# Kernel optimization log

Hardware: AMD Instinct MI355X
Metric: run time of the kernel (lower is better)

The kernel has to match this reference:

```python
import jax, jax.numpy as jnp
import numpy as np

D = 65
CHUNK = 64
K = 64
SCALE = D ** (-0.5)

def gelu(x):
    return jax.nn.gelu(x, approximate=False)  # torch nn.GELU default is exact erf

def setup_inputs() -> dict:
    key = jax.random.key(0)
    ks = jax.random.split(key, 16)
    B, N = 32, 16384
    s = SCALE
    return {
        "x": jax.random.normal(ks[0], (B, N, D), jnp.float32),
        # query_gen: Linear(D,D) -> GELU -> Linear(D, K*D)
        "Wq1": jax.random.normal(ks[1], (D, D), jnp.float32) * s,
        "bq1": jnp.zeros((D,), jnp.float32),
        "Wq2": jax.random.normal(ks[2], (D, K * D), jnp.float32) * s,
        "bq2": jnp.zeros((K * D,), jnp.float32),
        "Wk": jax.random.normal(ks[3], (D, D), jnp.float32) * s,
        "bk": jnp.zeros((D,), jnp.float32),
        "Wv": jax.random.normal(ks[4], (D, D), jnp.float32) * s,
        "bv": jnp.zeros((D,), jnp.float32),
        "cross_q": jax.random.normal(ks[5], (1, D), jnp.float32) * s,
        "pos_enc": jax.random.normal(ks[6], (1, CHUNK, D), jnp.float32) * s,
        "Wr": jax.random.normal(ks[7], (D, D), jnp.float32) * (1.0 / np.sqrt(D)),
        "br": jnp.zeros((D,), jnp.float32),
        "gamma": jnp.ones((D,), jnp.float32),
        "beta": jnp.zeros((D,), jnp.float32),
    }

def reference(x, Wq1, bq1, Wq2, bq2, Wk, bk, Wv, bv, cross_q, pos_enc, Wr, br, gamma, beta):
    B, N, d = x.shape
    nb = N // CHUNK  # N chosen divisible by CHUNK -> mask is all True, pad branch skipped

    # global average (mask all-ones => plain mean over N)
    gavg = jnp.mean(x, axis=1)  # [B, D]

    # queries: MLP on global average, reshape to [B, K, D], scaled
    q = (gelu(gavg @ Wq1 + bq1) @ Wq2 + bq2).reshape(B, K, d) * SCALE

    # keys / values: Linear + GELU, chunked, + positional encoding per chunk
    keys = gelu(x @ Wk + bk).reshape(B, nb, CHUNK, d) + pos_enc[None]      # [B,nb,C,D]
    values = gelu(x @ Wv + bv).reshape(B, nb, CHUNK, d) + pos_enc[None]    # [B,nb,C,D]

    # block-local attention (mask is all-True, masked_fill is a no-op)
    scores = jnp.einsum('bkd,bncd->bnkc', q, keys) * SCALE                 # [B,nb,K,C]
    w = jax.nn.softmax(scores, axis=-1)                                    # dropout = eval-mode identity
    blk = jnp.einsum('bnkc,bncd->bnkd', w, values)                         # [B,nb,K,D]
    blk = jnp.transpose(blk, (0, 2, 1, 3))                                 # [B,K,nb,D]

    # cross-block attention with a single learned query
    cs = jnp.einsum('d,bknd->bkn', cross_q[0], blk) * SCALE                # [B,K,nb]
    cw = jax.nn.softmax(cs, axis=-1)
    compressed = jnp.einsum('bkn,bknd->bkd', cw, blk)                      # [B,K,D]

    # residual + LayerNorm
    compressed = compressed + (gavg @ Wr + br)[:, None, :]
    mu = jnp.mean(compressed, axis=-1, keepdims=True)
    var = jnp.var(compressed, axis=-1, keepdims=True)
    return (compressed - mu) * jax.lax.rsqrt(var + 1e-5) * gamma + beta
```

## Files before the change

kernel.cpp:

```cpp
#include <hip/hip_runtime.h>
#include <hip/hip_bf16.h>

#define BATCH 32
#define NSEQ  16384
#define DDIM  65
#define CHUNK 64
#define KQ    64
#define NBLK  256
#define SCALE 0.12403473458920847f
#define BSTRIDE 68

typedef __bf16 bf16x8 __attribute__((ext_vector_type(8)));
typedef __bf16 bf16x4 __attribute__((ext_vector_type(4)));
typedef float  f32x4  __attribute__((ext_vector_type(4)));
#define MFMA16(a, b, c) __builtin_amdgcn_mfma_f32_16x16x32_bf16(a, b, c, 0, 0, 0)

__device__ __forceinline__ float gelu_exact(float v) {
    return 0.5f * v * (1.0f + erff(v * 0.7071067811865476f));
}

__device__ __forceinline__ float gelu_tanh(float x) {
    float x2 = x * x;
    float t  = 0.7978845608028654f * x * fmaf(0.044715f, x2, 1.0f);
    float e  = __expf(2.0f * t);
    float th = 1.0f - 2.0f * __builtin_amdgcn_rcpf(e + 1.0f);
    return 0.5f * x * (1.0f + th);
}

__device__ __forceinline__ void load_lds16(const void* g, void* l) {
    __builtin_amdgcn_global_load_lds(
        (const __attribute__((address_space(1))) unsigned int*)g,
        (__attribute__((address_space(3))) unsigned int*)l, 16, 0, 0);
}

__global__ __launch_bounds__(256) void k_prep(const float* __restrict__ Wk,
                                              const float* __restrict__ Wv,
                                              __bf16* __restrict__ WkT,
                                              __bf16* __restrict__ WvT) {
    int i = blockIdx.x * 256 + threadIdx.x;
    if (i >= 2 * 80 * 64) return;
    int m = i / 5120;
    int j = i - m * 5120;
    int d = j >> 6, e = j & 63;
    const float* W = m ? Wv : Wk;
    __bf16* T = m ? WvT : WkT;
    T[(size_t)d * 64 + e] = (d < DDIM) ? (__bf16)W[e * DDIM + d] : (__bf16)0.0f;
}

__global__ __launch_bounds__(256) void k_gavg(const float* __restrict__ x,
                                              float* __restrict__ partial,
                                              __bf16* __restrict__ xbf,
                                              float* __restrict__ x64g) {
    const int s = blockIdx.x;
    const int b = blockIdx.y;
    const int tid = threadIdx.x;
    const int w = tid >> 6, lane = tid & 63;
    const float* xb = x + (size_t)b * NSEQ * DDIM;
    const int n0 = s * 256;
    float acc = 0.f, acce = 0.f;
    #pragma unroll 4
    for (int i = 0; i < 64; ++i) {
        const int n = n0 + w + i * 4;
        const float* row = xb + (size_t)n * DDIM;
        const float v = row[lane];
        acc += v;
        xbf[((size_t)b * NSEQ + n) * 64 + (lane ^ ((n & 7) << 3))] = (__bf16)v;
        if (lane == 0) {
            const float ve = row[64];
            acce += ve;
            x64g[(size_t)b * NSEQ + n] = ve;
        }
    }
    __shared__ float part[4][DDIM];
    part[w][lane] = acc;
    if (lane == 0) part[w][64] = acce;
    __syncthreads();
    if (tid < DDIM) {
        partial[((size_t)b * 64 + s) * DDIM + tid] =
            part[0][tid] + part[1][tid] + part[2][tid] + part[3][tid];
    }
}

__global__ __launch_bounds__(256) void k_qgen1(const float* __restrict__ partial,
    const float* __restrict__ Wq1, const float* __restrict__ bq1,
    const float* __restrict__ Wr,  const float* __restrict__ br,
    float* __restrict__ h_out, float* __restrict__ r_out) {
    const int b = blockIdx.x, tid = threadIdx.x;
    __shared__ float g[DDIM];
    if (tid < DDIM) {
        float a = 0.f;
        const float* p = partial + (size_t)b * 64 * DDIM + tid;
        #pragma unroll 8
        for (int s = 0; s < 64; ++s) a += p[s * DDIM];
        g[tid] = a * (1.0f / 16384.0f);
    }
    __syncthreads();
    if (tid < DDIM) {
        float a = bq1[tid];
        for (int e = 0; e < DDIM; ++e) a += g[e] * Wq1[e * DDIM + tid];
        h_out[b * DDIM + tid] = gelu_exact(a);
    } else if (tid >= 128 && tid < 128 + DDIM) {
        const int d = tid - 128;
        float a = br[d];
        for (int e = 0; e < DDIM; ++e) a += g[e] * Wr[e * DDIM + d];
        r_out[b * DDIM + d] = a;
    }
}

__global__ __launch_bounds__(256) void k_qgen2(const float* __restrict__ h_in,
    const float* __restrict__ Wq2, const float* __restrict__ bq2,
    __bf16* __restrict__ qbf, float* __restrict__ q64) {
    const int b = blockIdx.y, tid = threadIdx.x;
    const int o = blockIdx.x * 256 + tid;
    __shared__ float h[DDIM];
    if (tid < DDIM) h[tid] = h_in[b * DDIM + tid];
    __syncthreads();
    if (o >= KQ * DDIM) return;
    float a = bq2[o];
    #pragma unroll 13
    for (int e = 0; e < DDIM; ++e) a += h[e] * Wq2[e * (KQ * DDIM) + o];
    a *= SCALE;
    const int k = o / DDIM, d = o - k * DDIM;
    if (d < 64) qbf[(size_t)b * 4096 + k * 64 + d] = (__bf16)a;
    else        q64[b * 64 + k] = a;
}

__global__ __launch_bounds__(256, 6) void k_attn(
    const __bf16* __restrict__ xbf, const float* __restrict__ x64g,
    const __bf16* __restrict__ qbf, const float* __restrict__ q64g,
    const __bf16* __restrict__ WkT, const __bf16* __restrict__ WvT,
    const float* __restrict__ Wk, const float* __restrict__ bkb,
    const float* __restrict__ Wv, const float* __restrict__ bvb,
    const float* __restrict__ pos, const float* __restrict__ cq,
    __bf16* __restrict__ blk_out, float* __restrict__ cs_out) {
    const int nb = blockIdx.x;
    const int b  = blockIdx.y;
    const int tid = threadIdx.x;
    const int lane = tid & 63, w = tid >> 6;
    const int l16 = lane & 15, quad = lane >> 4;

    __shared__ __align__(16) __bf16 xP[64 * 64];
    __shared__ __align__(16) __bf16 keysL[64 * 64];
    __shared__ __align__(16) __bf16 valsT[64 * 64];
    __shared__ __align__(16) __bf16 kcol64[64];
    __shared__ __align__(16) __bf16 vcol64[64];
    __shared__ float xs64[64];

    const int krow = w * 16 + l16;
    const __bf16* qr = qbf + (size_t)b * 4096 + krow * 64 + quad * 8;
    bf16x8 q0 = *(const bf16x8*)qr;
    bf16x8 q1 = *(const bf16x8*)(qr + 32);
    const float q64k = q64g[b * 64 + krow];

    {
        const char* xg = (const char*)(xbf + ((size_t)b * NSEQ + (size_t)nb * CHUNK) * 64);
        char* lp = (char*)xP;
        #pragma unroll
        for (int j = 0; j < 2; ++j) {
            const int o = j * 4096 + w * 1024;
            load_lds16(xg + o + lane * 16, lp + o);
        }
        if (tid < 64) xs64[tid] = x64g[(size_t)b * NSEQ + (size_t)nb * CHUNK + tid];
    }
    __syncthreads();

    {
        const int crow = w * 16 + l16;
        const int sw_c = (crow & 7) << 4;
        const char* xrow = (const char*)xP + crow * 128;
        bf16x8 x0 = *(const bf16x8*)(xrow + ((quad * 16) ^ sw_c));
        bf16x8 x1 = *(const bf16x8*)(xrow + ((quad * 16 + 64) ^ sw_c));
        const float xe_c = xs64[crow];
        const f32x4 z = {0.f, 0.f, 0.f, 0.f};

        f32x4 kacc[5];
        #pragma unroll
        for (int mt = 0; mt < 5; ++mt) {
            const __bf16* wr = WkT + (mt * 16 + l16) * 64 + quad * 8;
            kacc[mt] = MFMA16(*(const bf16x8*)wr, x0, z);
            kacc[mt] = MFMA16(*(const bf16x8*)(wr + 32), x1, kacc[mt]);
        }
        #pragma unroll
        for (int mt = 0; mt < 4; ++mt) {
            const int d0 = mt * 16 + quad * 4;
            bf16x4 kv;
            #pragma unroll
            for (int r = 0; r < 4; ++r) {
                const int d = d0 + r;
                const float pre = kacc[mt][r] + xe_c * Wk[64 * DDIM + d] + bkb[d];
                kv[r] = (__bf16)(gelu_tanh(pre) + pos[crow * DDIM + d]);
            }
            *(bf16x4*)((char*)keysL + crow * 128 + ((d0 * 2) ^ sw_c)) = kv;
        }
        if (quad == 0) {
            const float pre = kacc[4][0] + xe_c * Wk[64 * DDIM + 64] + bkb[64];
            kcol64[crow] = (__bf16)(gelu_tanh(pre) + pos[crow * DDIM + 64]);
        }

        f32x4 vacc[5];
        #pragma unroll
        for (int nt = 0; nt < 5; ++nt) {
            const __bf16* wr = WvT + (nt * 16 + l16) * 64 + quad * 8;
            vacc[nt] = MFMA16(x0, *(const bf16x8*)wr, z);
            vacc[nt] = MFMA16(x1, *(const bf16x8*)(wr + 32), vacc[nt]);
        }
        const int cv0 = w * 16 + quad * 4;
        float xe4[4];
        #pragma unroll
        for (int r = 0; r < 4; ++r) xe4[r] = xs64[cv0 + r];
        #pragma unroll
        for (int nt = 0; nt < 4; ++nt) {
            const int d = nt * 16 + l16;
            const float wv64d = Wv[64 * DDIM + d], bvd = bvb[d];
            bf16x4 vv;
            #pragma unroll
            for (int r = 0; r < 4; ++r) {
                const float pre = vacc[nt][r] + xe4[r] * wv64d + bvd;
                vv[r] = (__bf16)(gelu_tanh(pre) + pos[(cv0 + r) * DDIM + d]);
            }
            *(bf16x4*)((char*)valsT + d * 128 + ((cv0 * 2) ^ ((d & 7) << 4))) = vv;
        }
        if (l16 == 0) {
            const float wv64d = Wv[64 * DDIM + 64], bvd = bvb[64];
            bf16x4 vv;
            #pragma unroll
            for (int r = 0; r < 4; ++r) {
                const float pre = vacc[4][r] + xe4[r] * wv64d + bvd;
                vv[r] = (__bf16)(gelu_tanh(pre) + pos[(cv0 + r) * DDIM + 64]);
            }
            *(bf16x4*)((char*)vcol64 + cv0 * 2) = vv;
        }
    }
    __syncthreads();

    float inv_k, o64n;
    {
        const f32x4 z = {0.f, 0.f, 0.f, 0.f};
        float st[4][4];
        #pragma unroll
        for (int mt = 0; mt < 4; ++mt) {
            const int cA = mt * 16 + l16;
            const char* kr = (const char*)keysL + cA * 128;
            const int swc = (cA & 7) << 4;
            f32x4 s = MFMA16(*(const bf16x8*)(kr + ((quad * 16) ^ swc)), q0, z);
            s = MFMA16(*(const bf16x8*)(kr + ((quad * 16 + 64) ^ swc)), q1, s);
            bf16x4 k4 = *(const bf16x4*)((const char*)kcol64 + (mt * 16 + quad * 4) * 2);
            #pragma unroll
            for (int r = 0; r < 4; ++r)
                st[mt][r] = fmaf(q64k, (float)k4[r], s[r]) * SCALE;
        }
        float m = st[0][0];
        #pragma unroll
        for (int mt = 0; mt < 4; ++mt)
            #pragma unroll
            for (int r = 0; r < 4; ++r) m = fmaxf(m, st[mt][r]);
        m = fmaxf(m, __shfl_xor(m, 16));
        m = fmaxf(m, __shfl_xor(m, 32));
        float sum = 0.f;
        #pragma unroll
        for (int mt = 0; mt < 4; ++mt)
            #pragma unroll
            for (int r = 0; r < 4; ++r) {
                st[mt][r] = __expf(st[mt][r] - m);
                sum += st[mt][r];
            }
        sum += __shfl_xor(sum, 16);
        sum += __shfl_xor(sum, 32);
        inv_k = __builtin_amdgcn_rcpf(sum);

        const int swk = (krow & 7) << 4;
        char* prow = (char*)xP + krow * 128;
        #pragma unroll
        for (int mt = 0; mt < 4; ++mt) {
            bf16x4 p4;
            #pragma unroll
            for (int r = 0; r < 4; ++r) p4[r] = (__bf16)st[mt][r];
            *(bf16x4*)(prow + (((mt * 16 + quad * 4) * 2) ^ swk)) = p4;
        }

        float o = 0.f;
        #pragma unroll
        for (int mt = 0; mt < 4; ++mt) {
            bf16x4 v4 = *(const bf16x4*)((const char*)vcol64 + (mt * 16 + quad * 4) * 2);
            #pragma unroll
            for (int r = 0; r < 4; ++r) o = fmaf(st[mt][r], (float)v4[r], o);
        }
        o += __shfl_xor(o, 16);
        o += __shfl_xor(o, 32);
        o64n = o * inv_k;
        if (quad == 0)
            blk_out[(((size_t)b * NBLK + nb) * KQ + krow) * BSTRIDE + 64] = (__bf16)o64n;
    }

    {
        const f32x4 z = {0.f, 0.f, 0.f, 0.f};
        const int swk = (krow & 7) << 4;
        const char* prow = (const char*)xP + krow * 128;
        bf16x8 p0 = *(const bf16x8*)(prow + ((quad * 16) ^ swk));
        bf16x8 p1 = *(const bf16x8*)(prow + ((quad * 16 + 64) ^ swk));
        const size_t obase = (((size_t)b * NBLK + nb) * KQ + krow) * BSTRIDE;
        float csp = 0.f;
        #pragma unroll
        for (int mt = 0; mt < 4; ++mt) {
            const int dA = mt * 16 + l16;
            const char* vr = (const char*)valsT + dA * 128;
            const int swd = (dA & 7) << 4;
            f32x4 o = MFMA16(*(const bf16x8*)(vr + ((quad * 16) ^ swd)), p0, z);
            o = MFMA16(*(const bf16x8*)(vr + ((quad * 16 + 64) ^ swd)), p1, o);
            const int d0 = mt * 16 + quad * 4;
            bf16x4 o4;
            #pragma unroll
            for (int r = 0; r < 4; ++r) {
                o4[r] = (__bf16)(o[r] * inv_k);
                csp = fmaf(o[r], cq[d0 + r], csp);
            }
            *(bf16x4*)((char*)blk_out + (obase + d0) * 2) = o4;
        }
        csp += __shfl_xor(csp, 16);
        csp += __shfl_xor(csp, 32);
        if (quad == 0) {
            const float cs = (csp * inv_k + cq[64] * o64n) * SCALE;
            cs_out[((size_t)b * KQ + krow) * NBLK + nb] = cs;
        }
    }
}

__global__ __launch_bounds__(256) void k_cross(
    const __bf16* __restrict__ blk, const float* __restrict__ cs,
    const float* __restrict__ r, const float* __restrict__ gamma,
    const float* __restrict__ beta, float* __restrict__ out) {
    const int bk_ = blockIdx.x;
    const int b = bk_ >> 6;
    const int k = bk_ & 63;
    const int tid = threadIdx.x;
    const int w = tid >> 6, lane = tid & 63;

    __shared__ float ew[NBLK];
    __shared__ float red[4][DDIM];
    __shared__ float vv[DDIM];
    __shared__ float wredA[4];
    __shared__ float stats[2];

    const float v = cs[(size_t)bk_ * NBLK + tid];
    float m = v;
    for (int off = 32; off; off >>= 1) m = fmaxf(m, __shfl_down(m, off));
    if (lane == 0) wredA[w] = m;
    __syncthreads();
    m = fmaxf(fmaxf(wredA[0], wredA[1]), fmaxf(wredA[2], wredA[3]));
    const float e = __expf(v - m);
    ew[tid] = e;
    float s = e;
    for (int off = 32; off; off >>= 1) s += __shfl_down(s, off);
    __syncthreads();
    if (lane == 0) wredA[w] = s;
    __syncthreads();
    const float inv = 1.0f / (wredA[0] + wredA[1] + wredA[2] + wredA[3]);

    const __bf16* base = blk + ((size_t)b * NBLK * KQ + k) * BSTRIDE;
    float acc = 0.f, acce = 0.f;
    #pragma unroll 4
    for (int i = 0; i < 64; ++i) {
        const int n = w + i * 4;
        const __bf16* row = base + (size_t)n * (KQ * BSTRIDE);
        const float wgt = ew[n];
        acc  += wgt * (float)row[lane];
        acce += wgt * (float)row[64];
    }
    red[w][lane] = acc;
    if (lane == 0) red[w][64] = acce;
    __syncthreads();
    if (tid < DDIM) {
        vv[tid] = (red[0][tid] + red[1][tid] + red[2][tid] + red[3][tid]) * inv
                  + r[b * DDIM + tid];
    }
    __syncthreads();
    if (tid < 64) {
        float a  = vv[tid] + (tid == 0 ? vv[64] : 0.f);
        float sq = vv[tid] * vv[tid] + (tid == 0 ? vv[64] * vv[64] : 0.f);
        for (int off = 32; off; off >>= 1) {
            a  += __shfl_down(a, off);
            sq += __shfl_down(sq, off);
        }
        if (tid == 0) {
            const float mu  = a * (1.0f / DDIM);
            const float var = sq * (1.0f / DDIM) - mu * mu;
            stats[0] = mu;
            stats[1] = rsqrtf(var + 1e-5f);
        }
    }
    __syncthreads();
    if (tid < DDIM) {
        out[(size_t)bk_ * DDIM + tid] =
            (vv[tid] - stats[0]) * stats[1] * gamma[tid] + beta[tid];
    }
}

extern "C" void kernel_launch(void* const* d_in, const int* in_sizes, int n_in,
                              void* d_out, int out_size, void* d_ws, size_t ws_size,
                              hipStream_t stream) {
    const float* x    = (const float*)d_in[0];
    const float* Wq1  = (const float*)d_in[1];
    const float* bq1  = (const float*)d_in[2];
    const float* Wq2  = (const float*)d_in[3];
    const float* bq2  = (const float*)d_in[4];
    const float* Wk   = (const float*)d_in[5];
    const float* bk   = (const float*)d_in[6];
    const float* Wv   = (const float*)d_in[7];
    const float* bv   = (const float*)d_in[8];
    const float* cq   = (const float*)d_in[9];
    const float* pos  = (const float*)d_in[10];
    const float* Wr   = (const float*)d_in[11];
    const float* br   = (const float*)d_in[12];
    const float* gamma= (const float*)d_in[13];
    const float* beta = (const float*)d_in[14];
    float* out = (float*)d_out;

    char* w8 = (char*)d_ws;
    float*  partial = (float*)w8;
    float*  rres    = (float*)(w8 + 532480);
    float*  q64     = (float*)(w8 + 540800);
    float*  hbuf    = (float*)(w8 + 548992);
    float*  cs      = (float*)(w8 + 557312);
    __bf16* qbf     = (__bf16*)(w8 + 2654464);
    __bf16* WkT     = (__bf16*)(w8 + 2916608);
    __bf16* WvT     = (__bf16*)(w8 + 2926848);
    float*  x64     = (float*)(w8 + 2937088);
    __bf16* xbf     = (__bf16*)(w8 + 5034240);
    __bf16* blk     = (__bf16*)(w8 + 72143104);

    k_prep<<<40, 256, 0, stream>>>(Wk, Wv, WkT, WvT);
    k_gavg<<<dim3(64, BATCH), 256, 0, stream>>>(x, partial, xbf, x64);
    k_qgen1<<<BATCH, 256, 0, stream>>>(partial, Wq1, bq1, Wr, br, hbuf, rres);
    k_qgen2<<<dim3(17, BATCH), 256, 0, stream>>>(hbuf, Wq2, bq2, qbf, q64);
    k_attn<<<dim3(NBLK, BATCH), 256, 0, stream>>>(xbf, x64, qbf, q64, WkT, WvT,
                                                  Wk, bk, Wv, bv, pos, cq,
                                                  blk, cs);
    k_cross<<<BATCH * KQ, 256, 0, stream>>>(blk, cs, rres, gamma, beta, out);
}
```

Before: 432.3 us.

## Read fp32 x directly in attention kernel and relayout block outputs for cross pass

```diff
diff --git a/kernel.cpp b/kernel.cpp
--- a/kernel.cpp
+++ b/kernel.cpp
@@ -8,7 +8,6 @@
 #define KQ    64
 #define NBLK  256
 #define SCALE 0.12403473458920847f
-#define BSTRIDE 68
 
 typedef __bf16 bf16x8 __attribute__((ext_vector_type(8)));
 typedef __bf16 bf16x4 __attribute__((ext_vector_type(4)));
@@ -27,30 +26,42 @@
     return 0.5f * x * (1.0f + th);
 }
 
-__device__ __forceinline__ void load_lds16(const void* g, void* l) {
-    __builtin_amdgcn_global_load_lds(
-        (const __attribute__((address_space(1))) unsigned int*)g,
-        (__attribute__((address_space(3))) unsigned int*)l, 16, 0, 0);
-}
-
 __global__ __launch_bounds__(256) void k_prep(const float* __restrict__ Wk,
                                               const float* __restrict__ Wv,
+                                              const float* __restrict__ pos,
                                               __bf16* __restrict__ WkT,
-                                              __bf16* __restrict__ WvT) {
+                                              __bf16* __restrict__ WvT,
+                                              float* __restrict__ posK,
+                                              float* __restrict__ posV,
+                                              float* __restrict__ wkc,
+                                              float* __restrict__ wvc) {
     int i = blockIdx.x * 256 + threadIdx.x;
-    if (i >= 2 * 80 * 64) return;
-    int m = i / 5120;
-    int j = i - m * 5120;
-    int d = j >> 6, e = j & 63;
-    const float* W = m ? Wv : Wk;
-    __bf16* T = m ? WvT : WkT;
-    T[(size_t)d * 64 + e] = (d < DDIM) ? (__bf16)W[e * DDIM + d] : (__bf16)0.0f;
+    if (i < 10240) {
+        int m = i / 5120;
+        int j = i - m * 5120;
+        int d = j >> 6, e = j & 63;
+        const float* W = m ? Wv : Wk;
+        __bf16* T = m ? WvT : WkT;
+        T[(size_t)d * 64 + e] = (d < DDIM) ? (__bf16)W[e * DDIM + d] : (__bf16)0.0f;
+    } else if (i < 14592) {
+        int j = i - 10240;
+        int c = j / 68, d = j - c * 68;
+        posK[j] = (d < DDIM) ? pos[c * DDIM + d] : 0.f;
+    } else if (i < 19012) {
+        int j = i - 14592;
+        int d = j / 68, c = j - d * 68;
+        posV[j] = (d < DDIM && c < 64) ? pos[c * DDIM + d] : 0.f;
+    } else if (i < 19080) {
+        int d = i - 19012;
+        wkc[d] = (d < DDIM) ? Wk[64 * DDIM + d] : 0.f;
+    } else if (i < 19148) {
+        int d = i - 19080;
+        wvc[d] = (d < DDIM) ? Wv[64 * DDIM + d] : 0.f;
+    }
 }
 
 __global__ __launch_bounds__(256) void k_gavg(const float* __restrict__ x,
-                                              float* __restrict__ partial,
-                                              __bf16* __restrict__ xbf,
-                                              float* __restrict__ x64g) {
+                                              float* __restrict__ partial) {
     const int s = blockIdx.x;
     const int b = blockIdx.y;
     const int tid = threadIdx.x;
@@ -60,16 +71,9 @@
     float acc = 0.f, acce = 0.f;
     #pragma unroll 4
     for (int i = 0; i < 64; ++i) {
-        const int n = n0 + w + i * 4;
-        const float* row = xb + (size_t)n * DDIM;
-        const float v = row[lane];
-        acc += v;
-        xbf[((size_t)b * NSEQ + n) * 64 + (lane ^ ((n & 7) << 3))] = (__bf16)v;
-        if (lane == 0) {
-            const float ve = row[64];
-            acce += ve;
-            x64g[(size_t)b * NSEQ + n] = ve;
-        }
+        const float* row = xb + (size_t)(n0 + w + i * 4) * DDIM;
+        acc  += row[lane];
+        acce += row[64];
     }
     __shared__ float part[4][DDIM];
     part[w][lane] = acc;
@@ -125,14 +129,16 @@
     else        q64[b * 64 + k] = a;
 }
 
-__global__ __launch_bounds__(256, 6) void k_attn(
-    const __bf16* __restrict__ xbf, const float* __restrict__ x64g,
+__global__ __launch_bounds__(256, 5) void k_attn(
+    const float* __restrict__ x,
     const __bf16* __restrict__ qbf, const float* __restrict__ q64g,
     const __bf16* __restrict__ WkT, const __bf16* __restrict__ WvT,
-    const float* __restrict__ Wk, const float* __restrict__ bkb,
-    const float* __restrict__ Wv, const float* __restrict__ bvb,
-    const float* __restrict__ pos, const float* __restrict__ cq,
-    __bf16* __restrict__ blk_out, float* __restrict__ cs_out) {
+    const float* __restrict__ posK, const float* __restrict__ posV,
+    const float* __restrict__ wkc, const float* __restrict__ wvc,
+    const float* __restrict__ bkb, const float* __restrict__ bvb,
+    const float* __restrict__ cq,
+    __bf16* __restrict__ blk_out, __bf16* __restrict__ blk64_out,
+    float* __restrict__ cs_out) {
     const int nb = blockIdx.x;
     const int b  = blockIdx.y;
     const int tid = threadIdx.x;
@@ -153,14 +159,17 @@
     const float q64k = q64g[b * 64 + krow];
 
     {
-        const char* xg = (const char*)(xbf + ((size_t)b * NSEQ + (size_t)nb * CHUNK) * 64);
-        char* lp = (char*)xP;
-        #pragma unroll
-        for (int j = 0; j < 2; ++j) {
-            const int o = j * 4096 + w * 1024;
-            load_lds16(xg + o + lane * 16, lp + o);
-        }
-        if (tid < 64) xs64[tid] = x64g[(size_t)b * NSEQ + (size_t)nb * CHUNK + tid];
+        const int c = tid >> 2, g = tid & 3;
+        const float* xrow = x + ((size_t)b * NSEQ + (size_t)nb * CHUNK + c) * DDIM;
+        const int sw = (c & 7) << 4;
+        char* dst = (char*)xP + c * 128;
+        #pragma unroll
+        for (int j = 0; j < 16; ++j) {
+            const int e = g + 4 * j;
+            const float v = xrow[e];
+            *(__bf16*)(dst + ((((e >> 3) << 4) ^ sw) + (e & 7) * 2)) = (__bf16)v;
+        }
+        if (g == 0) xs64[c] = xrow[64];
     }
     __syncthreads();
 
@@ -183,18 +192,20 @@
         #pragma unroll
         for (int mt = 0; mt < 4; ++mt) {
             const int d0 = mt * 16 + quad * 4;
+            const f32x4 pk  = *(const f32x4*)(posK + crow * 68 + d0);
+            const f32x4 wk4 = *(const f32x4*)(wkc + d0);
+            const f32x4 bk4 = *(const f32x4*)(bkb + d0);
             bf16x4 kv;
             #pragma unroll
             for (int r = 0; r < 4; ++r) {
-                const int d = d0 + r;
-                const float pre = kacc[mt][r] + xe_c * Wk[64 * DDIM + d] + bkb[d];
-                kv[r] = (__bf16)(gelu_tanh(pre) + pos[crow * DDIM + d]);
+                const float pre = kacc[mt][r] + xe_c * wk4[r] + bk4[r];
+                kv[r] = (__bf16)(gelu_tanh(pre) + pk[r]);
             }
             *(bf16x4*)((char*)keysL + crow * 128 + ((d0 * 2) ^ sw_c)) = kv;
         }
         if (quad == 0) {
-            const float pre = kacc[4][0] + xe_c * Wk[64 * DDIM + 64] + bkb[64];
-            kcol64[crow] = (__bf16)(gelu_tanh(pre) + pos[crow * DDIM + 64]);
+            const float pre = kacc[4][0] + xe_c * wkc[64] + bkb[64];
+            kcol64[crow] = (__bf16)(gelu_tanh(pre) + posK[crow * 68 + 64]);
         }
 
         f32x4 vacc[5];
@@ -211,22 +222,24 @@
         #pragma unroll
         for (int nt = 0; nt < 4; ++nt) {
             const int d = nt * 16 + l16;
-            const float wv64d = Wv[64 * DDIM + d], bvd = bvb[d];
+            const float wvd = wvc[d], bvd = bvb[d];
+            const f32x4 pv = *(const f32x4*)(posV + d * 68 + cv0);
             bf16x4 vv;
             #pragma unroll
             for (int r = 0; r < 4; ++r) {
-                const float pre = vacc[nt][r] + xe4[r] * wv64d + bvd;
-                vv[r] = (__bf16)(gelu_tanh(pre) + pos[(cv0 + r) * DDIM + d]);
+                const float pre = vacc[nt][r] + xe4[r] * wvd + bvd;
+                vv[r] = (__bf16)(gelu_tanh(pre) + pv[r]);
             }
             *(bf16x4*)((char*)valsT + d * 128 + ((cv0 * 2) ^ ((d & 7) << 4))) = vv;
         }
         if (l16 == 0) {
-            const float wv64d = Wv[64 * DDIM + 64], bvd = bvb[64];
+            const float wvd = wvc[64], bvd = bvb[64];
+            const f32x4 pv = *(const f32x4*)(posV + 64 * 68 + cv0);
             bf16x4 vv;
             #pragma unroll
             for (int r = 0; r < 4; ++r) {
-                const float pre = vacc[4][r] + xe4[r] * wv64d + bvd;
-                vv[r] = (__bf16)(gelu_tanh(pre) + pos[(cv0 + r) * DDIM + 64]);
+                const float pre = vacc[4][r] + xe4[r] * wvd + bvd;
+                vv[r] = (__bf16)(gelu_tanh(pre) + pv[r]);
             }
             *(bf16x4*)((char*)vcol64 + cv0 * 2) = vv;
         }
@@ -289,7 +302,7 @@
         o += __shfl_xor(o, 32);
         o64n = o * inv_k;
         if (quad == 0)
-            blk_out[(((size_t)b * NBLK + nb) * KQ + krow) * BSTRIDE + 64] = (__bf16)o64n;
+            blk64_out[((size_t)b * KQ + krow) * NBLK + nb] = (__bf16)o64n;
     }
 
     {
@@ -298,7 +311,8 @@
         const char* prow = (const char*)xP + krow * 128;
         bf16x8 p0 = *(const bf16x8*)(prow + ((quad * 16) ^ swk));
         bf16x8 p1 = *(const bf16x8*)(prow + ((quad * 16 + 64) ^ swk));
-        const size_t obase = (((size_t)b * NBLK + nb) * KQ + krow) * BSTRIDE;
+        const size_t obase = (((size_t)b * KQ + krow) * NBLK + nb) * 64;
+        const float cq64 = cq[64];
         float csp = 0.f;
         #pragma unroll
         for (int mt = 0; mt < 4; ++mt) {
@@ -308,30 +322,31 @@
             f32x4 o = MFMA16(*(const bf16x8*)(vr + ((quad * 16) ^ swd)), p0, z);
             o = MFMA16(*(const bf16x8*)(vr + ((quad * 16 + 64) ^ swd)), p1, o);
             const int d0 = mt * 16 + quad * 4;
+            const f32x4 cq4 = *(const f32x4*)(cq + d0);
             bf16x4 o4;
             #pragma unroll
             for (int r = 0; r < 4; ++r) {
                 o4[r] = (__bf16)(o[r] * inv_k);
-                csp = fmaf(o[r], cq[d0 + r], csp);
+                csp = fmaf(o[r], cq4[r], csp);
             }
             *(bf16x4*)((char*)blk_out + (obase + d0) * 2) = o4;
         }
         csp += __shfl_xor(csp, 16);
         csp += __shfl_xor(csp, 32);
         if (quad == 0) {
-            const float cs = (csp * inv_k + cq[64] * o64n) * SCALE;
+            const float cs = (csp * inv_k + cq64 * o64n) * SCALE;
             cs_out[((size_t)b * KQ + krow) * NBLK + nb] = cs;
         }
     }
 }
 
 __global__ __launch_bounds__(256) void k_cross(
-    const __bf16* __restrict__ blk, const float* __restrict__ cs,
+    const __bf16* __restrict__ blk, const __bf16* __restrict__ blk64,
+    const float* __restrict__ cs,
     const float* __restrict__ r, const float* __restrict__ gamma,
     const float* __restrict__ beta, float* __restrict__ out) {
     const int bk_ = blockIdx.x;
     const int b = bk_ >> 6;
-    const int k = bk_ & 63;
     const int tid = threadIdx.x;
     const int w = tid >> 6, lane = tid & 63;
 
@@ -356,15 +371,16 @@
     __syncthreads();
     const float inv = 1.0f / (wredA[0] + wredA[1] + wredA[2] + wredA[3]);
 
-    const __bf16* base = blk + ((size_t)b * NBLK * KQ + k) * BSTRIDE;
+    const __bf16* base = blk + (size_t)bk_ * NBLK * 64;
+    const __bf16* b64p = blk64 + (size_t)bk_ * NBLK;
     float acc = 0.f, acce = 0.f;
     #pragma unroll 4
     for (int i = 0; i < 64; ++i) {
         const int n = w + i * 4;
-        const __bf16* row = base + (size_t)n * (KQ * BSTRIDE);
+        const __bf16* row = base + n * 64;
         const float wgt = ew[n];
         acc  += wgt * (float)row[lane];
-        acce += wgt * (float)row[64];
+        acce += wgt * (float)b64p[n];
     }
     red[w][lane] = acc;
     if (lane == 0) red[w][64] = acce;
@@ -424,16 +440,19 @@
     __bf16* qbf     = (__bf16*)(w8 + 2654464);
     __bf16* WkT     = (__bf16*)(w8 + 2916608);
     __bf16* WvT     = (__bf16*)(w8 + 2926848);
-    float*  x64     = (float*)(w8 + 2937088);
-    __bf16* xbf     = (__bf16*)(w8 + 5034240);
-    __bf16* blk     = (__bf16*)(w8 + 72143104);
-
-    k_prep<<<40, 256, 0, stream>>>(Wk, Wv, WkT, WvT);
-    k_gavg<<<dim3(64, BATCH), 256, 0, stream>>>(x, partial, xbf, x64);
+    float*  posK    = (float*)(w8 + 2937088);
+    float*  posV    = (float*)(w8 + 2954496);
+    float*  wkc     = (float*)(w8 + 2972176);
+    float*  wvc     = (float*)(w8 + 2972448);
+    __bf16* blk     = (__bf16*)(w8 + 2972720);
+    __bf16* blk64   = (__bf16*)(w8 + 70081584);
+
+    k_prep<<<75, 256, 0, stream>>>(Wk, Wv, pos, WkT, WvT, posK, posV, wkc, wvc);
+    k_gavg<<<dim3(64, BATCH), 256, 0, stream>>>(x, partial);
     k_qgen1<<<BATCH, 256, 0, stream>>>(partial, Wq1, bq1, Wr, br, hbuf, rres);
     k_qgen2<<<dim3(17, BATCH), 256, 0, stream>>>(hbuf, Wq2, bq2, qbf, q64);
-    k_attn<<<dim3(NBLK, BATCH), 256, 0, stream>>>(xbf, x64, qbf, q64, WkT, WvT,
-                                                  Wk, bk, Wv, bv, pos, cq,
-                                                  blk, cs);
-    k_cross<<<BATCH * KQ, 256, 0, stream>>>(blk, cs, rres, gamma, beta, out);
-}
+    k_attn<<<dim3(NBLK, BATCH), 256, 0, stream>>>(x, qbf, q64, WkT, WvT,
+                                                  posK, posV, wkc, wvc,
+                                                  bk, bv, cq, blk, blk64, cs);
+    k_cross<<<BATCH * KQ, 256, 0, stream>>>(blk, blk64, cs, rres, gamma, beta, out);
+}
```

Result: faster. 387.4 us (-10.4%).
